# Kernel optimization log

Measured on AMD Instinct MI355X. Metric: run time of the kernel, lower is better.

## Reference

```python
import jax, jax.numpy as jnp
import numpy as np

TEMPERATURE = 0.1
B, D, A = 8192, 256, 4


def setup_inputs() -> dict:
    key = jax.random.key(0)
    k1, k2 = jax.random.split(key)
    # scale by 1/sqrt(D) so dot products are O(1) and exp(sim/T) is finite
    embeddings = jax.random.normal(k1, (B, D), dtype=jnp.float32) / jnp.sqrt(jnp.float32(D))
    labels = jax.random.randint(k2, (B, A), 0, 6, dtype=jnp.int64)
    return {"embeddings": embeddings, "labels": labels}


def reference(embeddings, labels):
    b = embeddings.shape[0]
    # [B, B] similarity scaled by temperature
    sim = jnp.matmul(embeddings, embeddings.T) / TEMPERATURE
    # positive mask: ANY aspect matches (vectorized over aspects), diagonal zeroed
    pos_mask = jnp.any(labels[:, None, :] == labels[None, :, :], axis=-1)
    pos_mask = pos_mask & ~jnp.eye(b, dtype=bool)
    pos_mask = pos_mask.astype(sim.dtype)

    exp_sim = jnp.exp(sim)
    positive_sim = jnp.sum(exp_sim * pos_mask, axis=1)            # [B]
    all_sim = jnp.sum(exp_sim, axis=1) - jnp.diagonal(exp_sim)   # [B]

    valid = positive_sim > 0
    pos_safe = jnp.where(valid, positive_sim, 1.0)
    all_safe = jnp.where(valid, all_sim, 1.0)
    row_loss = jnp.where(valid, -jnp.log(pos_safe / (all_safe + 1e-8)), 0.0)

    num_pos = jnp.sum(valid.astype(sim.dtype))
    loss = jnp.where(num_pos > 0, jnp.sum(row_loss) / jnp.maximum(num_pos, 1.0), 0.0)
    return loss
```

## Files before the change

### kernel.cpp

```cpp
#include <hip/hip_runtime.h>
#include <stdint.h>

typedef short short8 __attribute__((ext_vector_type(8)));
typedef float f32x4 __attribute__((ext_vector_type(4)));
typedef float f32x2 __attribute__((ext_vector_type(2)));

#define B_TOTAL 8192
#define DDIM 256
#define BM 256
#define BN 64
#define NSPLIT 16
#define COLS_PER (B_TOTAL / NSPLIT)
#define ITERS (COLS_PER / BN)
#define NBLOCKS ((B_TOTAL / BM) * NSPLIT)
#define SCALE_HALF 3.79828546f
#define LN2F 0.6931471805599453f

typedef __attribute__((address_space(3))) char lds_char;
typedef __attribute__((address_space(1))) const char gbl_char;

__device__ __forceinline__ unsigned short f2bf(float f) {
  unsigned int u = __builtin_bit_cast(unsigned int, f);
  u = (u + 0x7FFFu + ((u >> 16) & 1u)) >> 16;
  return (unsigned short)u;
}

__global__ __launch_bounds__(256) void prep_all(
    const float* __restrict__ E, const int* __restrict__ lab,
    unsigned short* __restrict__ Eb, unsigned int* __restrict__ plab,
    float* __restrict__ posAll) {
  const int t = blockIdx.x * 256 + threadIdx.x;
  const float4* s4 = (const float4*)E + (size_t)t * 2;
  float4 v0 = s4[0], v1 = s4[1];
  short8 o;
  o[0] = (short)f2bf(v0.x * SCALE_HALF); o[1] = (short)f2bf(v0.y * SCALE_HALF);
  o[2] = (short)f2bf(v0.z * SCALE_HALF); o[3] = (short)f2bf(v0.w * SCALE_HALF);
  o[4] = (short)f2bf(v1.x * SCALE_HALF); o[5] = (short)f2bf(v1.y * SCALE_HALF);
  o[6] = (short)f2bf(v1.z * SCALE_HALF); o[7] = (short)f2bf(v1.w * SCALE_HALF);
  *(short8*)(Eb + (size_t)t * 8) = o;
  if (t < B_TOTAL) {
    int4 l = ((const int4*)lab)[t];
    plab[t] = (1u << ((unsigned)l.x & 31u))
            | (1u << (((unsigned)l.y & 31u) + 6u))
            | (1u << (((unsigned)l.z & 31u) + 12u))
            | (1u << (((unsigned)l.w & 31u) + 18u));
  }
  if (t < 2 * B_TOTAL) posAll[t] = 0.0f;
}

struct __align__(16) SMem {
  char btile[2][BN * DDIM * 2];
  unsigned int plab_all[COLS_PER];
};

template <int DIAG>
__device__ __forceinline__ void epi_n(
    const f32x4 (&acc)[2], int n, int colbase, int itBN, int l15,
    const unsigned int (&pi)[2][4], const int (&irow)[2][4],
    const unsigned int* __restrict__ plab_all,
    f32x2 (&pos2)[2][2], f32x2 (&all2)[2][2]) {
  const int j = colbase + n * 16 + l15;
  const unsigned int hj = plab_all[itBN + n * 16 + l15];
#pragma unroll
  for (int m = 0; m < 2; ++m) {
    float e[4];
#pragma unroll
    for (int q = 0; q < 4; ++q) {
      float v = __builtin_amdgcn_exp2f(acc[m][q]);
      if (DIAG) { if (j == irow[m][q]) v = 0.0f; }
      e[q] = v;
    }
    f32x2 p01 = { (pi[m][0] & hj) ? e[0] : 0.0f, (pi[m][1] & hj) ? e[1] : 0.0f };
    f32x2 p23 = { (pi[m][2] & hj) ? e[2] : 0.0f, (pi[m][3] & hj) ? e[3] : 0.0f };
    all2[m][0] += (f32x2){e[0], e[1]};
    all2[m][1] += (f32x2){e[2], e[3]};
    pos2[m][0] += p01;
    pos2[m][1] += p23;
  }
}

template <int DIAG>
__device__ __forceinline__ void iter_body(
    const char* __restrict__ btile, const unsigned int* __restrict__ plab_all,
    const short8 (&afrag)[2][8], const unsigned int (&pi)[2][4],
    const int (&irow)[2][4], int colbase, int itBN, int l15, int l4,
    f32x2 (&pos2)[2][2], f32x2 (&all2)[2][2]) {
  auto kloop = [&](int n, f32x4 (&acc)[2]) {
    acc[0] = (f32x4){0.f, 0.f, 0.f, 0.f};
    acc[1] = (f32x4){0.f, 0.f, 0.f, 0.f};
    const unsigned int rr = (unsigned int)(n * 16 + l15);
#pragma unroll
    for (int k = 0; k < 8; ++k) {
      const unsigned int s = ((unsigned int)(k * 4 + l4)) ^ (rr & 7u);
      short8 b = *(const short8*)(btile + rr * 512u + s * 16u);
      acc[0] = __builtin_amdgcn_mfma_f32_16x16x32_bf16(afrag[0][k], b, acc[0], 0, 0, 0);
      acc[1] = __builtin_amdgcn_mfma_f32_16x16x32_bf16(afrag[1][k], b, acc[1], 0, 0, 0);
    }
  };
  f32x4 accA[2], accB[2];
  __builtin_amdgcn_s_setprio(1);
  kloop(0, accA);
  kloop(1, accB);
  epi_n<DIAG>(accA, 0, colbase, itBN, l15, pi, irow, plab_all, pos2, all2);
  kloop(2, accA);
  epi_n<DIAG>(accB, 1, colbase, itBN, l15, pi, irow, plab_all, pos2, all2);
  kloop(3, accB);
  __builtin_amdgcn_s_setprio(0);
  epi_n<DIAG>(accA, 2, colbase, itBN, l15, pi, irow, plab_all, pos2, all2);
  epi_n<DIAG>(accB, 3, colbase, itBN, l15, pi, irow, plab_all, pos2, all2);
}

__global__ __launch_bounds__(512, 2) void main_kernel(
    const unsigned short* __restrict__ Eb, const unsigned int* __restrict__ plab,
    float* __restrict__ posArr, float* __restrict__ allArr) {
  __shared__ SMem sm;
  const int tid = threadIdx.x;
  const int lane = tid & 63;
  const int wid = tid >> 6;
  const int l15 = lane & 15;
  const int l4 = lane >> 4;
  const int rb = (int)blockIdx.x & 31;
  const int cs = (int)blockIdx.x >> 5;
  const int rowbase = rb * BM;
  const int colstart = cs * COLS_PER;

  auto stage = [&](int bufi, int cb) {
#pragma unroll
    for (int q = 0; q < 4; ++q) {
      const unsigned int base = (unsigned int)q * 8192u + (unsigned int)wid * 1024u;
      const unsigned int L = base + (unsigned int)lane * 16u;
      const unsigned int r = L >> 9;
      const unsigned int s = (L >> 4) & 31u;
      const unsigned int c = s ^ (r & 7u);
      const char* src = (const char*)(Eb + (size_t)(cb + (int)r) * DDIM + c * 8);
      char* dst = sm.btile[bufi] + base;
      __builtin_amdgcn_global_load_lds((gbl_char*)src, (lds_char*)dst, 16, 0, 0);
    }
  };

  stage(0, colstart);

  short8 afrag[2][8];
#pragma unroll
  for (int m = 0; m < 2; ++m) {
    const int row = rowbase + wid * 32 + m * 16 + l15;
    const unsigned short* rp = Eb + (size_t)row * DDIM + l4 * 8;
#pragma unroll
    for (int k = 0; k < 8; ++k) afrag[m][k] = *(const short8*)(rp + k * 32);
  }

  sm.plab_all[tid] = plab[colstart + tid];

  unsigned int pi[2][4];
  int irow[2][4];
#pragma unroll
  for (int m = 0; m < 2; ++m)
#pragma unroll
    for (int q = 0; q < 4; ++q) {
      const int i = rowbase + wid * 32 + m * 16 + l4 * 4 + q;
      irow[m][q] = i;
      pi[m][q] = plab[i];
    }

  asm volatile("s_waitcnt lgkmcnt(0)" ::: "memory");
  __builtin_amdgcn_sched_barrier(0);

  f32x2 pos2[2][2] = {};
  f32x2 all2[2][2] = {};

  for (int it = 0; it < ITERS; ++it) {
    const int colbase = colstart + it * BN;
    const int cur = it & 1;

    if (it + 1 < ITERS) {
      stage(cur ^ 1, colbase + BN);
      asm volatile("s_waitcnt vmcnt(4)" ::: "memory");
    } else {
      asm volatile("s_waitcnt vmcnt(0)" ::: "memory");
    }
    __builtin_amdgcn_s_barrier();
    __builtin_amdgcn_sched_barrier(0);

    const bool hasDiag = (colbase < rowbase + BM) && (rowbase < colbase + BN);
    if (hasDiag)
      iter_body<1>(sm.btile[cur], sm.plab_all, afrag, pi, irow,
                   colbase, it * BN, l15, l4, pos2, all2);
    else
      iter_body<0>(sm.btile[cur], sm.plab_all, afrag, pi, irow,
                   colbase, it * BN, l15, l4, pos2, all2);

    __builtin_amdgcn_s_barrier();
    __builtin_amdgcn_sched_barrier(0);
  }

#pragma unroll
  for (int m = 0; m < 2; ++m)
#pragma unroll
    for (int q = 0; q < 4; ++q) {
      float p = pos2[m][q >> 1][q & 1], al = all2[m][q >> 1][q & 1];
      p += __shfl_xor(p, 1); p += __shfl_xor(p, 2);
      p += __shfl_xor(p, 4); p += __shfl_xor(p, 8);
      al += __shfl_xor(al, 1); al += __shfl_xor(al, 2);
      al += __shfl_xor(al, 4); al += __shfl_xor(al, 8);
      if (l15 == 0) {
        atomicAdd(&posArr[irow[m][q]], p);
        atomicAdd(&allArr[irow[m][q]], al);
      }
    }
}

__global__ __launch_bounds__(1024) void finalize_kernel(
    const float* __restrict__ posArr, const float* __restrict__ allArr,
    float* __restrict__ out) {
  float ls = 0.f, cnt = 0.f;
#pragma unroll
  for (int k = 0; k < B_TOTAL / 1024; ++k) {
    const int i = threadIdx.x + (k << 10);
    const float p = posArr[i];
    const float a = allArr[i];
    if (p > 0.f) {
      ls += (__builtin_amdgcn_logf(a + 1e-8f) - __builtin_amdgcn_logf(p)) * LN2F;
      cnt += 1.f;
    }
  }
#pragma unroll
  for (int msk = 1; msk < 64; msk <<= 1) {
    ls += __shfl_xor(ls, msk);
    cnt += __shfl_xor(cnt, msk);
  }
  __shared__ float sls[16], scnt[16];
  const int w = threadIdx.x >> 6;
  if ((threadIdx.x & 63) == 0) { sls[w] = ls; scnt[w] = cnt; }
  __syncthreads();
  if (threadIdx.x == 0) {
    float L = 0.f, C = 0.f;
    for (int i = 0; i < 16; ++i) { L += sls[i]; C += scnt[i]; }
    out[0] = (C > 0.f) ? L / fmaxf(C, 1.f) : 0.f;
  }
}

extern "C" void kernel_launch(void* const* d_in, const int* in_sizes, int n_in,
                              void* d_out, int out_size, void* d_ws, size_t ws_size,
                              hipStream_t stream) {
  const float* E = (const float*)d_in[0];
  const int* lab = (const int*)d_in[1];
  float* out = (float*)d_out;
  char* ws = (char*)d_ws;

  unsigned short* Eb = (unsigned short*)ws;
  unsigned int* plab = (unsigned int*)(ws + 4u * 1024u * 1024u);
  float* posArr = (float*)(ws + 4u * 1024u * 1024u + 32u * 1024u);
  float* allArr = posArr + B_TOTAL;

  prep_all<<<1024, 256, 0, stream>>>(E, lab, Eb, plab, posArr);
  main_kernel<<<NBLOCKS, 512, 0, stream>>>(Eb, plab, posArr, allArr);
  finalize_kernel<<<1, 1024, 0, stream>>>(posArr, allArr, out);
}
```

Measured before the change: 113.1 us.

## Switch similarity GEMM from bf16 to fp8 MFMA with permuted fp8 layout

Embeddings are quantized to fp8 in the prep kernel instead of bf16, stored in a k-permuted layout so each lane loads 16 bytes covering two MFMA k-steps, and the main GEMM uses fp8 MFMA. This halves LDS tile size and global traffic and uses the higher-throughput fp8 matrix path. The cost is reduced precision of the dot products, and exp of sim/T amplifies those errors, which could affect loss accuracy.

```diff
diff --git a/kernel.cpp b/kernel.cpp
--- a/kernel.cpp
+++ b/kernel.cpp
@@ -4,6 +4,7 @@
 typedef short short8 __attribute__((ext_vector_type(8)));
 typedef float f32x4 __attribute__((ext_vector_type(4)));
 typedef float f32x2 __attribute__((ext_vector_type(2)));
+typedef long lng2 __attribute__((ext_vector_type(2)));
 
 #define B_TOTAL 8192
 #define DDIM 256
@@ -19,25 +20,25 @@
 typedef __attribute__((address_space(3))) char lds_char;
 typedef __attribute__((address_space(1))) const char gbl_char;
 
-__device__ __forceinline__ unsigned short f2bf(float f) {
-  unsigned int u = __builtin_bit_cast(unsigned int, f);
-  u = (u + 0x7FFFu + ((u >> 16) & 1u)) >> 16;
-  return (unsigned short)u;
-}
-
 __global__ __launch_bounds__(256) void prep_all(
     const float* __restrict__ E, const int* __restrict__ lab,
-    unsigned short* __restrict__ Eb, unsigned int* __restrict__ plab,
+    unsigned char* __restrict__ Eb8, unsigned int* __restrict__ plab,
     float* __restrict__ posAll) {
   const int t = blockIdx.x * 256 + threadIdx.x;
   const float4* s4 = (const float4*)E + (size_t)t * 2;
   float4 v0 = s4[0], v1 = s4[1];
-  short8 o;
-  o[0] = (short)f2bf(v0.x * SCALE_HALF); o[1] = (short)f2bf(v0.y * SCALE_HALF);
-  o[2] = (short)f2bf(v0.z * SCALE_HALF); o[3] = (short)f2bf(v0.w * SCALE_HALF);
-  o[4] = (short)f2bf(v1.x * SCALE_HALF); o[5] = (short)f2bf(v1.y * SCALE_HALF);
-  o[6] = (short)f2bf(v1.z * SCALE_HALF); o[7] = (short)f2bf(v1.w * SCALE_HALF);
-  *(short8*)(Eb + (size_t)t * 8) = o;
+  unsigned int d0 = (unsigned int)__builtin_amdgcn_cvt_pk_fp8_f32(
+      v0.x * SCALE_HALF, v0.y * SCALE_HALF, 0, false);
+  d0 = (unsigned int)__builtin_amdgcn_cvt_pk_fp8_f32(
+      v0.z * SCALE_HALF, v0.w * SCALE_HALF, (int)d0, true);
+  unsigned int d1 = (unsigned int)__builtin_amdgcn_cvt_pk_fp8_f32(
+      v1.x * SCALE_HALF, v1.y * SCALE_HALF, 0, false);
+  d1 = (unsigned int)__builtin_amdgcn_cvt_pk_fp8_f32(
+      v1.z * SCALE_HALF, v1.w * SCALE_HALF, (int)d1, true);
+  const int row = t >> 5, j = t & 31;
+  unsigned char* orow = Eb8 + (size_t)row * DDIM + ((j & 3) * 64 + (j >> 2) * 8);
+  *(unsigned long long*)orow =
+      (unsigned long long)d0 | ((unsigned long long)d1 << 32);
   if (t < B_TOTAL) {
     int4 l = ((const int4*)lab)[t];
     plab[t] = (1u << ((unsigned)l.x & 31u))
@@ -49,7 +50,7 @@
 }
 
 struct __align__(16) SMem {
-  char btile[2][BN * DDIM * 2];
+  char btile[2][BN * DDIM];
   unsigned int plab_all[COLS_PER];
 };
 
@@ -82,7 +83,7 @@
 template <int DIAG>
 __device__ __forceinline__ void iter_body(
     const char* __restrict__ btile, const unsigned int* __restrict__ plab_all,
-    const short8 (&afrag)[2][8], const unsigned int (&pi)[2][4],
+    const long (&afrag)[2][8], const unsigned int (&pi)[2][4],
     const int (&irow)[2][4], int colbase, int itBN, int l15, int l4,
     f32x2 (&pos2)[2][2], f32x2 (&all2)[2][2]) {
   auto kloop = [&](int n, f32x4 (&acc)[2]) {
@@ -90,11 +91,18 @@
     acc[1] = (f32x4){0.f, 0.f, 0.f, 0.f};
     const unsigned int rr = (unsigned int)(n * 16 + l15);
 #pragma unroll
-    for (int k = 0; k < 8; ++k) {
-      const unsigned int s = ((unsigned int)(k * 4 + l4)) ^ (rr & 7u);
-      short8 b = *(const short8*)(btile + rr * 512u + s * 16u);
-      acc[0] = __builtin_amdgcn_mfma_f32_16x16x32_bf16(afrag[0][k], b, acc[0], 0, 0, 0);
-      acc[1] = __builtin_amdgcn_mfma_f32_16x16x32_bf16(afrag[1][k], b, acc[1], 0, 0, 0);
+    for (int kw8 = 0; kw8 < 4; ++kw8) {
+      const unsigned int c = (unsigned int)(l4 * 4 + kw8);
+      const unsigned int s = c ^ (rr & 7u);
+      lng2 b2 = *(const lng2*)(btile + rr * 256u + s * 16u);
+      acc[0] = __builtin_amdgcn_mfma_f32_16x16x32_fp8_fp8(
+          afrag[0][kw8 * 2], b2[0], acc[0], 0, 0, 0);
+      acc[1] = __builtin_amdgcn_mfma_f32_16x16x32_fp8_fp8(
+          afrag[1][kw8 * 2], b2[0], acc[1], 0, 0, 0);
+      acc[0] = __builtin_amdgcn_mfma_f32_16x16x32_fp8_fp8(
+          afrag[0][kw8 * 2 + 1], b2[1], acc[0], 0, 0, 0);
+      acc[1] = __builtin_amdgcn_mfma_f32_16x16x32_fp8_fp8(
+          afrag[1][kw8 * 2 + 1], b2[1], acc[1], 0, 0, 0);
     }
   };
   f32x4 accA[2], accB[2];
@@ -111,7 +119,7 @@
 }
 
 __global__ __launch_bounds__(512, 2) void main_kernel(
-    const unsigned short* __restrict__ Eb, const unsigned int* __restrict__ plab,
+    const unsigned char* __restrict__ Eb8, const unsigned int* __restrict__ plab,
     float* __restrict__ posArr, float* __restrict__ allArr) {
   __shared__ SMem sm;
   const int tid = threadIdx.x;
@@ -126,13 +134,13 @@
 
   auto stage = [&](int bufi, int cb) {
 #pragma unroll
-    for (int q = 0; q < 4; ++q) {
+    for (int q = 0; q < 2; ++q) {
       const unsigned int base = (unsigned int)q * 8192u + (unsigned int)wid * 1024u;
       const unsigned int L = base + (unsigned int)lane * 16u;
-      const unsigned int r = L >> 9;
-      const unsigned int s = (L >> 4) & 31u;
+      const unsigned int r = L >> 8;
+      const unsigned int s = (L >> 4) & 15u;
       const unsigned int c = s ^ (r & 7u);
-      const char* src = (const char*)(Eb + (size_t)(cb + (int)r) * DDIM + c * 8);
+      const char* src = (const char*)(Eb8 + (size_t)(cb + (int)r) * DDIM + c * 16);
       char* dst = sm.btile[bufi] + base;
       __builtin_amdgcn_global_load_lds((gbl_char*)src, (lds_char*)dst, 16, 0, 0);
     }
@@ -140,13 +148,17 @@
 
   stage(0, colstart);
 
-  short8 afrag[2][8];
+  long afrag[2][8];
 #pragma unroll
   for (int m = 0; m < 2; ++m) {
     const int row = rowbase + wid * 32 + m * 16 + l15;
-    const unsigned short* rp = Eb + (size_t)row * DDIM + l4 * 8;
-#pragma unroll
-    for (int k = 0; k < 8; ++k) afrag[m][k] = *(const short8*)(rp + k * 32);
+    const char* rp = (const char*)Eb8 + (size_t)row * DDIM + l4 * 64;
+#pragma unroll
+    for (int kw8 = 0; kw8 < 4; ++kw8) {
+      lng2 t = *(const lng2*)(rp + kw8 * 16);
+      afrag[m][kw8 * 2] = t[0];
+      afrag[m][kw8 * 2 + 1] = t[1];
+    }
   }
 
   sm.plab_all[tid] = plab[colstart + tid];
@@ -162,7 +174,8 @@
       pi[m][q] = plab[i];
     }
 
-  asm volatile("s_waitcnt lgkmcnt(0)" ::: "memory");
+  asm volatile("s_waitcnt vmcnt(0) lgkmcnt(0)" ::: "memory");
+  __builtin_amdgcn_s_barrier();
   __builtin_amdgcn_sched_barrier(0);
 
   f32x2 pos2[2][2] = {};
@@ -174,7 +187,7 @@
 
     if (it + 1 < ITERS) {
       stage(cur ^ 1, colbase + BN);
-      asm volatile("s_waitcnt vmcnt(4)" ::: "memory");
+      asm volatile("s_waitcnt vmcnt(2)" ::: "memory");
     } else {
       asm volatile("s_waitcnt vmcnt(0)" ::: "memory");
     }
@@ -247,12 +260,12 @@
   float* out = (float*)d_out;
   char* ws = (char*)d_ws;
 
-  unsigned short* Eb = (unsigned short*)ws;
-  unsigned int* plab = (unsigned int*)(ws + 4u * 1024u * 1024u);
-  float* posArr = (float*)(ws + 4u * 1024u * 1024u + 32u * 1024u);
+  unsigned char* Eb8 = (unsigned char*)ws;
+  unsigned int* plab = (unsigned int*)(ws + 2u * 1024u * 1024u);
+  float* posArr = (float*)(ws + 2u * 1024u * 1024u + 32u * 1024u);
   float* allArr = posArr + B_TOTAL;
 
-  prep_all<<<1024, 256, 0, stream>>>(E, lab, Eb, plab, posArr);
-  main_kernel<<<NBLOCKS, 512, 0, stream>>>(Eb, plab, posArr, allArr);
+  prep_all<<<1024, 256, 0, stream>>>(E, lab, Eb8, plab, posArr);
+  main_kernel<<<NBLOCKS, 512, 0, stream>>>(Eb8, plab, posArr, allArr);
   finalize_kernel<<<1, 1024, 0, stream>>>(posArr, allArr, out);
 }
```

Measured after the change: 102.4 us. -9.5%, faster.
